# Optimization experiments

Hardware: AMD Instinct MI355X
Metric: run time of the kernel (lower is better)

## Reference

```python
import jax, jax.numpy as jnp
import numpy as np

NEG_SLOPE = 0.1
N, D = 8192, 256


def setup_inputs() -> dict:
    key = jax.random.key(0)
    ks = jax.random.split(key, 7)
    head = jax.random.normal(ks[0], (N, D), dtype=jnp.float32)
    dependent = jax.random.normal(ks[1], (N, D), dtype=jnp.float32)
    alpha = jax.random.uniform(ks[2], (N, N), dtype=jnp.float32)
    # parameters (torch.rand init -> uniform [0,1))
    agg_weight_head = jax.random.uniform(ks[3], (D, D), dtype=jnp.float32)
    agg_weight_dependent = jax.random.uniform(ks[4], (D, D), dtype=jnp.float32)
    comb_weight_head = jax.random.uniform(ks[5], (D, D), dtype=jnp.float32)
    comb_weight_dependent = jax.random.uniform(ks[6], (D, D), dtype=jnp.float32)
    return {
        "head": head, "dependent": dependent, "alpha": alpha,
        "agg_weight_head": agg_weight_head,
        "agg_weight_dependent": agg_weight_dependent,
        "comb_weight_head": comb_weight_head,
        "comb_weight_dependent": comb_weight_dependent,
    }


def reference(head, dependent, alpha, agg_weight_head, agg_weight_dependent,
              comb_weight_head, comb_weight_dependent):
    # Double loop over j != i is equivalent to dense matmuls with the
    # diagonal contribution subtracted:
    #   head_agg[i]  = sum_j alpha[j,i]*head[j] + alpha[i,j]*dependent[j]  (j != i)
    #   dep_agg[i]   = sum_j alpha[i,j]*head[j] + alpha[j,i]*dependent[j]  (j != i)
    diag = jnp.diagonal(alpha)[:, None]                      # [N,1]
    hd_sum = head + dependent                                # [N,D]
    head_agg = alpha.T @ head + alpha @ dependent - diag * hd_sum
    dep_agg = alpha @ head + alpha.T @ dependent - diag * hd_sum
    head_out = jax.nn.leaky_relu(head_agg @ agg_weight_head + head @ comb_weight_head,
                                 negative_slope=NEG_SLOPE)
    dep_out = jax.nn.leaky_relu(dep_agg @ agg_weight_dependent + dependent @ comb_weight_dependent,
                                negative_slope=NEG_SLOPE)
    return (head_out, dep_out)
```

## Files before the change

### kernel.cpp

```cpp
#include <hip/hip_runtime.h>

#define NN 8192
#define DD 256
#define ND_ (NN * DD)

#define NEG_SLOPE 0.1f

typedef _Float16 half8 __attribute__((ext_vector_type(8)));
typedef _Float16 half4 __attribute__((ext_vector_type(4)));
typedef float f32x4 __attribute__((ext_vector_type(4)));
typedef float f32x16 __attribute__((ext_vector_type(16)));

__device__ __forceinline__ void ld_g2l16(const void* g, void* l) {
    __builtin_amdgcn_global_load_lds(
        (const __attribute__((address_space(1))) void*)g,
        (__attribute__((address_space(3))) void*)l, 16, 0, 0);
}

__device__ __forceinline__ unsigned pkhalf2(_Float16 a, _Float16 b) {
    unsigned short ua = __builtin_bit_cast(unsigned short, a);
    unsigned short ub = __builtin_bit_cast(unsigned short, b);
    return (unsigned)ua | ((unsigned)ub << 16);
}

__global__ __launch_bounds__(256, 2)
void prep_split_kernel(const float* __restrict__ h, const float* __restrict__ d,
                       _Float16* __restrict__ uS_hi, _Float16* __restrict__ vS_hi) {
    __shared__ float s_h[64 * 68];
    __shared__ float s_d[64 * 68];
    const int b  = blockIdx.x;
    const int kt = b >> 2;
    const int ct = b & 3;
    const int k0 = kt * 64;
    const int c0 = ct * 64;
    const int t  = threadIdx.x;

#pragma unroll
    for (int e = 0; e < 4; ++e) {
        int idx = e * 256 + t;
        int r   = idx >> 4;
        int c4  = (idx & 15) << 2;
        float4 hv = *(const float4*)&h[(size_t)(k0 + r) * DD + c0 + c4];
        float4 dv = *(const float4*)&d[(size_t)(k0 + r) * DD + c0 + c4];
        *(float4*)&s_h[r * 68 + c4] = hv;
        *(float4*)&s_d[r * 68 + c4] = dv;
    }
    __syncthreads();

#pragma unroll
    for (int e = 0; e < 2; ++e) {
        int idx = e * 256 + t;
        int c   = idx >> 3;
        int seg = idx & 7;
        half8 uh, vh;
#pragma unroll
        for (int m = 0; m < 8; ++m) {
            float hh = s_h[(seg * 8 + m) * 68 + c];
            float dd = s_d[(seg * 8 + m) * 68 + c];
            uh[m] = (_Float16)(hh + dd);
            vh[m] = (_Float16)(hh - dd);
        }
        int    cg   = c0 + c;
        int    kb   = kt * 2 + (seg >> 2);
        int    slot = (seg & 3) ^ ((cg >> 1) & 3);
        size_t go   = (size_t)kb * 8192 + (size_t)cg * 32 + slot * 8;
        *(half8*)&uS_hi[go] = uh;
        *(half8*)&vS_hi[go] = vh;
    }
}

__global__ __launch_bounds__(512, 4)
void agg_mfma_kernel(const float* __restrict__ alpha,
                     const _Float16* __restrict__ uS_hi, const _Float16* __restrict__ vS_hi,
                     _Float16* __restrict__ Pbuf,
                     _Float16* __restrict__ Qbuf) {
    __shared__ __align__(16) unsigned char smem[53248];
    _Float16* sS0  = (_Float16*)smem;
    _Float16* sD0  = (_Float16*)(smem + 5120);
    _Float16* sS1  = (_Float16*)(smem + 10240);
    _Float16* sD1  = (_Float16*)(smem + 15360);
    _Float16* sBu0 = (_Float16*)(smem + 20480);
    _Float16* sBv0 = (_Float16*)(smem + 28672);
    _Float16* sBu1 = (_Float16*)(smem + 36864);
    _Float16* sBv1 = (_Float16*)(smem + 45056);

    const int raw   = blockIdx.x;
    const int khalf = raw & 1;
    const int cb    = (raw >> 3) & 1;
    const int rb    = ((raw >> 1) & 3) | ((raw >> 4) << 2);
    const int I0    = rb * 64;
    const int C0    = cb * 128;
    const int t     = threadIdx.x;
    const int w     = t >> 6;
    const int lane  = t & 63;

    const bool isP = (w < 4);
    const int  cw  = w & 3;

    const _Float16* aP0 = isP ? sS0 : sD0;
    const _Float16* aP1 = isP ? sS1 : sD1;
    const _Float16* b0  = isP ? sBu0 : sBv0;
    const _Float16* b1  = isP ? sBu1 : sBv1;

    f32x16 acc0, acc1;
#pragma unroll
    for (int r = 0; r < 16; ++r) { acc0[r] = 0.f; acc1[r] = 0.f; }

    const int rbase = t & 15;
    const int kp    = (t >> 4) & 15;
    const int dup   = t >> 8;
    const int row0  = rbase + 32 * dup;
    const int lrow  = lane & 31;
    const int lk    = (lane >> 5) << 3;
    const int kbase = khalf * (NN / 2);
    const int c_local = cw * 32 + lrow;

#define LOAD_ALPHA(S, IT)                                                        \
    {                                                                            \
        const int kk0 = kbase + (IT) * 64 + 2 * kp;                              \
        size_t c0off = (size_t)kk0 * NN + I0;                                    \
        S##c00 = alpha[c0off + row0];                                            \
        S##c01 = alpha[c0off + NN + row0];                                       \
        S##c10 = alpha[c0off + row0 + 16];                                       \
        S##c11 = alpha[c0off + NN + row0 + 16];                                  \
        size_t c1off = c0off + (size_t)32 * NN;                                  \
        S##d00 = alpha[c1off + row0];                                            \
        S##d01 = alpha[c1off + NN + row0];                                       \
        S##d10 = alpha[c1off + row0 + 16];                                       \
        S##d11 = alpha[c1off + NN + row0 + 16];                                  \
        S##r00 = *(const float2*)&alpha[(size_t)(I0 + row0) * NN + kk0];         \
        S##r10 = *(const float2*)&alpha[(size_t)(I0 + row0 + 16) * NN + kk0];    \
        S##r01 = *(const float2*)&alpha[(size_t)(I0 + row0) * NN + kk0 + 32];    \
        S##r11 = *(const float2*)&alpha[(size_t)(I0 + row0 + 16) * NN + kk0 + 32]; \
    }

    float Ac00, Ac01, Ac10, Ac11, Ad00, Ad01, Ad10, Ad11;
    float2 Ar00, Ar10, Ar01, Ar11;
    float Bc00, Bc01, Bc10, Bc11, Bd00, Bd01, Bd10, Bd11;
    float2 Br00, Br10, Br01, Br11;
    float Cc00, Cc01, Cc10, Cc11, Cd00, Cd01, Cd10, Cd11;
    float2 Cr00, Cr10, Cr01, Cr11;
    float Nc00, Nc01, Nc10, Nc11, Nd00, Nd01, Nd10, Nd11;
    float2 Nr00, Nr10, Nr01, Nr11;

    LOAD_ALPHA(A, 0)
    LOAD_ALPHA(B, 1)
    LOAD_ALPHA(C, 2)

    for (int it = 0; it < 64; ++it) {
        unsigned su0_0 = pkhalf2((_Float16)(Ac00 + Ar00.x), (_Float16)(Ac01 + Ar00.y));
        unsigned du0_0 = pkhalf2((_Float16)(Ac00 - Ar00.x), (_Float16)(Ac01 - Ar00.y));
        unsigned su1_0 = pkhalf2((_Float16)(Ac10 + Ar10.x), (_Float16)(Ac11 + Ar10.y));
        unsigned du1_0 = pkhalf2((_Float16)(Ac10 - Ar10.x), (_Float16)(Ac11 - Ar10.y));
        unsigned su0_1 = pkhalf2((_Float16)(Ad00 + Ar01.x), (_Float16)(Ad01 + Ar01.y));
        unsigned du0_1 = pkhalf2((_Float16)(Ad00 - Ar01.x), (_Float16)(Ad01 - Ar01.y));
        unsigned su1_1 = pkhalf2((_Float16)(Ad10 + Ar11.x), (_Float16)(Ad11 + Ar11.y));
        unsigned du1_1 = pkhalf2((_Float16)(Ad10 - Ar11.x), (_Float16)(Ad11 - Ar11.y));

        __syncthreads();

        ((unsigned*)sS0)[row0 * 20 + kp]        = su0_0;
        ((unsigned*)sS0)[(row0 + 16) * 20 + kp] = su1_0;
        ((unsigned*)sD0)[row0 * 20 + kp]        = du0_0;
        ((unsigned*)sD0)[(row0 + 16) * 20 + kp] = du1_0;
        ((unsigned*)sS1)[row0 * 20 + kp]        = su0_1;
        ((unsigned*)sS1)[(row0 + 16) * 20 + kp] = su1_1;
        ((unsigned*)sD1)[row0 * 20 + kp]        = du0_1;
        ((unsigned*)sD1)[(row0 + 16) * 20 + kp] = du1_1;

        {
            size_t gb0 = (size_t)(khalf * 128 + it * 2) * 8192 + cb * 4096 +
                         (size_t)(w * 512 + lane * 8);
            ld_g2l16(uS_hi + gb0, (unsigned char*)sBu0 + w * 1024);
            ld_g2l16(vS_hi + gb0, (unsigned char*)sBv0 + w * 1024);
            ld_g2l16(uS_hi + gb0 + 8192, (unsigned char*)sBu1 + w * 1024);
            ld_g2l16(vS_hi + gb0 + 8192, (unsigned char*)sBv1 + w * 1024);
        }
        __builtin_amdgcn_sched_barrier(0);

        LOAD_ALPHA(N, ((it + 3) & 63))
        __builtin_amdgcn_sched_barrier(0);

        asm volatile("s_waitcnt vmcnt(12)" ::: "memory");
        asm volatile("s_waitcnt lgkmcnt(0)" ::: "memory");
        __builtin_amdgcn_s_barrier();
        __builtin_amdgcn_sched_barrier(0);

        __builtin_amdgcn_s_setprio(1);
#pragma unroll
        for (int s = 0; s < 2; ++s) {
            int gd = s * 2 + (lane >> 5);
            int sl = gd ^ ((c_local >> 1) & 3);
            int bi = c_local * 32 + sl * 8;
            half8 aH0 = *(const half8*)&aP0[(lrow) * 40 + s * 16 + lk];
            half8 aH1 = *(const half8*)&aP0[(32 + lrow) * 40 + s * 16 + lk];
            half8 bH  = *(const half8*)&b0[bi];
            acc0 = __builtin_amdgcn_mfma_f32_32x32x16_f16(aH0, bH, acc0, 0, 0, 0);
            acc1 = __builtin_amdgcn_mfma_f32_32x32x16_f16(aH1, bH, acc1, 0, 0, 0);
        }
#pragma unroll
        for (int s = 0; s < 2; ++s) {
            int gd = s * 2 + (lane >> 5);
            int sl = gd ^ ((c_local >> 1) & 3);
            int bi = c_local * 32 + sl * 8;
            half8 aH0 = *(const half8*)&aP1[(lrow) * 40 + s * 16 + lk];
            half8 aH1 = *(const half8*)&aP1[(32 + lrow) * 40 + s * 16 + lk];
            half8 bH  = *(const half8*)&b1[bi];
            acc0 = __builtin_amdgcn_mfma_f32_32x32x16_f16(aH0, bH, acc0, 0, 0, 0);
            acc1 = __builtin_amdgcn_mfma_f32_32x32x16_f16(aH1, bH, acc1, 0, 0, 0);
        }
        __builtin_amdgcn_s_setprio(0);

        Ac00 = Bc00; Ac01 = Bc01; Ac10 = Bc10; Ac11 = Bc11;
        Ad00 = Bd00; Ad01 = Bd01; Ad10 = Bd10; Ad11 = Bd11;
        Ar00 = Br00; Ar10 = Br10; Ar01 = Br01; Ar11 = Br11;
        Bc00 = Cc00; Bc01 = Cc01; Bc10 = Cc10; Bc11 = Cc11;
        Bd00 = Cd00; Bd01 = Cd01; Bd10 = Cd10; Bd11 = Cd11;
        Br00 = Cr00; Br10 = Cr10; Br01 = Cr01; Br11 = Cr11;
        Cc00 = Nc00; Cc01 = Nc01; Cc10 = Nc10; Cc11 = Nc11;
        Cd00 = Nd00; Cd01 = Nd01; Cd10 = Nd10; Cd11 = Nd11;
        Cr00 = Nr00; Cr10 = Nr10; Cr01 = Nr01; Cr11 = Nr11;
    }
#undef LOAD_ALPHA

    _Float16* dst = (isP ? Pbuf : Qbuf) + (size_t)khalf * ND_;
    const int colw = C0 + cw * 32 + (lane & 31);
#pragma unroll
    for (int reg = 0; reg < 16; ++reg) {
        int rr = (reg & 3) + ((reg >> 2) << 3) + ((lane >> 5) << 2);
        dst[(size_t)(I0 + rr) * DD + colw]      = (_Float16)acc0[reg];
        dst[(size_t)(I0 + 32 + rr) * DD + colw] = (_Float16)acc1[reg];
    }
}

__global__ __launch_bounds__(256, 2)
void stageB_kernel(const _Float16* __restrict__ Pbuf, const _Float16* __restrict__ Qbuf,
                   const float* __restrict__ head, const float* __restrict__ dep,
                   const float* __restrict__ alpha,
                   const float* __restrict__ Wah, const float* __restrict__ Wad,
                   const float* __restrict__ Wch, const float* __restrict__ Wcd,
                   float* __restrict__ out) {
    __shared__ float smem2[12544];
    __shared__ float s_dg[64];
    float* s_x  = smem2;
    float* s_y  = smem2 + 2176;
    float* s_w1 = smem2 + 4352;
    float* s_w2 = smem2 + 8448;

    int b   = blockIdx.x;
    int sel = b >> 8;
    int rem = b & 255;
    int rb  = rem >> 1;
    int cb  = rem & 1;
    int I0  = rb * 64;
    int C0  = cb * 128;

    const float* Y  = sel ? dep : head;
    const float* W1 = sel ? Wad : Wah;
    const float* W2 = sel ? Wcd : Wch;
    float* dst = out + sel * ND_;

    int t  = threadIdx.x;
    int rg = t & 15, cg = t >> 4;
    int r0 = rg * 4, c0 = cg * 8;

    if (t < 64) s_dg[t] = alpha[(size_t)(I0 + t) * NN + I0 + t];

    float acc[4][8];
#pragma unroll
    for (int i = 0; i < 4; ++i)
#pragma unroll
        for (int j = 0; j < 8; ++j) acc[i][j] = 0.0f;

    for (int it = 0; it < 8; ++it) {
        int k0 = it * 32;
        __syncthreads();
#pragma unroll
        for (int e = 0; e < 2; ++e) {
            int idx = e * 256 + t;
            int r   = idx >> 3;
            int k4  = (idx & 7) << 2;
            size_t go = (size_t)(I0 + r) * DD + k0 + k4;
            half4 p0 = *(const half4*)&Pbuf[go];
            half4 p1 = *(const half4*)&Pbuf[ND_ + go];
            half4 q0 = *(const half4*)&Qbuf[go];
            half4 q1 = *(const half4*)&Qbuf[ND_ + go];
            float4 hv = *(const float4*)&head[go];
            float4 dv = *(const float4*)&dep[go];
            float dgv = s_dg[r];
            float hj[4] = {hv.x, hv.y, hv.z, hv.w};
            float dj[4] = {dv.x, dv.y, dv.z, dv.w};
#pragma unroll
            for (int j = 0; j < 4; ++j) {
                float Pv = (float)p0[j] + (float)p1[j];
                float Qv = (float)q0[j] + (float)q1[j];
                float uu = hj[j] + dj[j];
                float x  = (sel ? 0.5f * (Pv - Qv) : 0.5f * (Pv + Qv)) - dgv * uu;
                s_x[(k4 + j) * 68 + r] = x;
                s_y[(k4 + j) * 68 + r] = sel ? dj[j] : hj[j];
            }
        }
#pragma unroll
        for (int e = 0; e < 4; ++e) {
            int idx = e * 256 + t;
            int kkk = idx >> 5;
            int c4  = (idx & 31) << 2;
            *(float4*)&s_w1[kkk * 128 + c4] =
                *(const float4*)&W1[(size_t)(k0 + kkk) * DD + C0 + c4];
            *(float4*)&s_w2[kkk * 128 + c4] =
                *(const float4*)&W2[(size_t)(k0 + kkk) * DD + C0 + c4];
        }
        __syncthreads();
#pragma unroll 8
        for (int k = 0; k < 32; ++k) {
            float4 xv = *(const float4*)&s_x[k * 68 + r0];
            float4 yv = *(const float4*)&s_y[k * 68 + r0];
            float4 wa = *(const float4*)&s_w1[k * 128 + c0];
            float4 wb = *(const float4*)&s_w1[k * 128 + c0 + 4];
            float4 wc = *(const float4*)&s_w2[k * 128 + c0];
            float4 wd = *(const float4*)&s_w2[k * 128 + c0 + 4];
            float xs[4]  = {xv.x, xv.y, xv.z, xv.w};
            float ys[4]  = {yv.x, yv.y, yv.z, yv.w};
            float w1s[8] = {wa.x, wa.y, wa.z, wa.w, wb.x, wb.y, wb.z, wb.w};
            float w2s[8] = {wc.x, wc.y, wc.z, wc.w, wd.x, wd.y, wd.z, wd.w};
#pragma unroll
            for (int i = 0; i < 4; ++i)
#pragma unroll
                for (int j = 0; j < 8; ++j)
                    acc[i][j] += xs[i] * w1s[j] + ys[i] * w2s[j];
        }
    }

#pragma unroll
    for (int i = 0; i < 4; ++i) {
#pragma unroll
        for (int jv = 0; jv < 2; ++jv) {
            float4 o;
            float v0 = acc[i][4 * jv + 0];
            float v1 = acc[i][4 * jv + 1];
            float v2 = acc[i][4 * jv + 2];
            float v3 = acc[i][4 * jv + 3];
            o.x = v0 >= 0.0f ? v0 : NEG_SLOPE * v0;
            o.y = v1 >= 0.0f ? v1 : NEG_SLOPE * v1;
            o.z = v2 >= 0.0f ? v2 : NEG_SLOPE * v2;
            o.w = v3 >= 0.0f ? v3 : NEG_SLOPE * v3;
            *(float4*)&dst[(size_t)(I0 + r0 + i) * DD + C0 + c0 + 4 * jv] = o;
        }
    }
}

extern "C" void kernel_launch(void* const* d_in, const int* in_sizes, int n_in,
                              void* d_out, int out_size, void* d_ws, size_t ws_size,
                              hipStream_t stream) {
    const float* head  = (const float*)d_in[0];
    const float* dep   = (const float*)d_in[1];
    const float* alpha = (const float*)d_in[2];
    const float* Wah   = (const float*)d_in[3];
    const float* Wad   = (const float*)d_in[4];
    const float* Wch   = (const float*)d_in[5];
    const float* Wcd   = (const float*)d_in[6];
    float* out = (float*)d_out;

    _Float16* ws    = (_Float16*)d_ws;
    _Float16* uS_hi = ws;
    _Float16* vS_hi = ws + (size_t)ND_;
    _Float16* Pbuf  = ws + (size_t)2 * ND_;
    _Float16* Qbuf  = ws + (size_t)4 * ND_;

    prep_split_kernel<<<512, 256, 0, stream>>>(head, dep, uS_hi, vS_hi);
    agg_mfma_kernel<<<512, 512, 0, stream>>>(alpha, uS_hi, vS_hi, Pbuf, Qbuf);
    stageB_kernel<<<512, 256, 0, stream>>>(Pbuf, Qbuf, head, dep, alpha,
                                           Wah, Wad, Wch, Wcd, out);
}
```

Baseline: 314.8 us.

## Enlarge agg row tile to 128 and split K four ways

The aggregation kernel now covers 128 rows per block instead of 64, using four accumulators per wave so each B tile loaded from LDS feeds more MFMAs. K is split into quarters rather than halves, which doubles the partial P/Q buffers and makes stageB sum four partials. The alpha prefetch depth drops from three iterations ahead to one, with a full vmcnt(0) wait at the top of each iteration. The costs are more LDS per block (73 KB), more registers, less latency hiding on alpha loads, and extra partial-sum traffic through the workspace.

```diff
diff --git a/kernel.cpp b/kernel.cpp
--- a/kernel.cpp
+++ b/kernel.cpp
@@ -74,25 +74,25 @@
                      const _Float16* __restrict__ uS_hi, const _Float16* __restrict__ vS_hi,
                      _Float16* __restrict__ Pbuf,
                      _Float16* __restrict__ Qbuf) {
-    __shared__ __align__(16) unsigned char smem[53248];
+    __shared__ __align__(16) unsigned char smem[73728];
     _Float16* sS0  = (_Float16*)smem;
-    _Float16* sD0  = (_Float16*)(smem + 5120);
-    _Float16* sS1  = (_Float16*)(smem + 10240);
-    _Float16* sD1  = (_Float16*)(smem + 15360);
-    _Float16* sBu0 = (_Float16*)(smem + 20480);
-    _Float16* sBv0 = (_Float16*)(smem + 28672);
-    _Float16* sBu1 = (_Float16*)(smem + 36864);
-    _Float16* sBv1 = (_Float16*)(smem + 45056);
-
-    const int raw   = blockIdx.x;
-    const int khalf = raw & 1;
-    const int cb    = (raw >> 3) & 1;
-    const int rb    = ((raw >> 1) & 3) | ((raw >> 4) << 2);
-    const int I0    = rb * 64;
-    const int C0    = cb * 128;
-    const int t     = threadIdx.x;
-    const int w     = t >> 6;
-    const int lane  = t & 63;
+    _Float16* sD0  = (_Float16*)(smem + 10240);
+    _Float16* sS1  = (_Float16*)(smem + 20480);
+    _Float16* sD1  = (_Float16*)(smem + 30720);
+    _Float16* sBu0 = (_Float16*)(smem + 40960);
+    _Float16* sBv0 = (_Float16*)(smem + 49152);
+    _Float16* sBu1 = (_Float16*)(smem + 57344);
+    _Float16* sBv1 = (_Float16*)(smem + 65536);
+
+    const int raw  = blockIdx.x;
+    const int kq   = raw & 3;
+    const int cb   = (raw >> 2) & 1;
+    const int rb   = raw >> 3;
+    const int I0   = rb * 128;
+    const int C0   = cb * 128;
+    const int t    = threadIdx.x;
+    const int w    = t >> 6;
+    const int lane = t & 63;
 
     const bool isP = (w < 4);
     const int  cw  = w & 3;
@@ -102,74 +102,88 @@
     const _Float16* b0  = isP ? sBu0 : sBv0;
     const _Float16* b1  = isP ? sBu1 : sBv1;
 
-    f32x16 acc0, acc1;
-#pragma unroll
-    for (int r = 0; r < 16; ++r) { acc0[r] = 0.f; acc1[r] = 0.f; }
-
-    const int rbase = t & 15;
+    f32x16 acc0, acc1, acc2, acc3;
+#pragma unroll
+    for (int r = 0; r < 16; ++r) { acc0[r] = 0.f; acc1[r] = 0.f; acc2[r] = 0.f; acc3[r] = 0.f; }
+
+    const int q     = t & 15;
     const int kp    = (t >> 4) & 15;
     const int dup   = t >> 8;
-    const int row0  = rbase + 32 * dup;
+    const int row0  = q + 16 * (4 * dup + 0);
+    const int row1  = q + 16 * (4 * dup + 1);
+    const int row2  = q + 16 * (4 * dup + 2);
+    const int row3  = q + 16 * (4 * dup + 3);
     const int lrow  = lane & 31;
     const int lk    = (lane >> 5) << 3;
-    const int kbase = khalf * (NN / 2);
+    const int kbase = kq * 2048;
     const int c_local = cw * 32 + lrow;
 
-#define LOAD_ALPHA(S, IT)                                                        \
-    {                                                                            \
-        const int kk0 = kbase + (IT) * 64 + 2 * kp;                              \
-        size_t c0off = (size_t)kk0 * NN + I0;                                    \
-        S##c00 = alpha[c0off + row0];                                            \
-        S##c01 = alpha[c0off + NN + row0];                                       \
-        S##c10 = alpha[c0off + row0 + 16];                                       \
-        S##c11 = alpha[c0off + NN + row0 + 16];                                  \
-        size_t c1off = c0off + (size_t)32 * NN;                                  \
-        S##d00 = alpha[c1off + row0];                                            \
-        S##d01 = alpha[c1off + NN + row0];                                       \
-        S##d10 = alpha[c1off + row0 + 16];                                       \
-        S##d11 = alpha[c1off + NN + row0 + 16];                                  \
-        S##r00 = *(const float2*)&alpha[(size_t)(I0 + row0) * NN + kk0];         \
-        S##r10 = *(const float2*)&alpha[(size_t)(I0 + row0 + 16) * NN + kk0];    \
-        S##r01 = *(const float2*)&alpha[(size_t)(I0 + row0) * NN + kk0 + 32];    \
-        S##r11 = *(const float2*)&alpha[(size_t)(I0 + row0 + 16) * NN + kk0 + 32]; \
-    }
-
-    float Ac00, Ac01, Ac10, Ac11, Ad00, Ad01, Ad10, Ad11;
-    float2 Ar00, Ar10, Ar01, Ar11;
-    float Bc00, Bc01, Bc10, Bc11, Bd00, Bd01, Bd10, Bd11;
-    float2 Br00, Br10, Br01, Br11;
-    float Cc00, Cc01, Cc10, Cc11, Cd00, Cd01, Cd10, Cd11;
-    float2 Cr00, Cr10, Cr01, Cr11;
-    float Nc00, Nc01, Nc10, Nc11, Nd00, Nd01, Nd10, Nd11;
-    float2 Nr00, Nr10, Nr01, Nr11;
+#define LOAD_ALPHA(S, IT)                                                          \
+    {                                                                              \
+        const int kk0 = kbase + (IT) * 64 + 2 * kp;                                \
+        size_t z0 = (size_t)kk0 * NN + I0;                                         \
+        size_t z1 = z0 + (size_t)32 * NN;                                          \
+        S##c000 = alpha[z0 + row0];      S##c010 = alpha[z0 + NN + row0];          \
+        S##c001 = alpha[z0 + row1];      S##c011 = alpha[z0 + NN + row1];          \
+        S##c002 = alpha[z0 + row2];      S##c012 = alpha[z0 + NN + row2];          \
+        S##c003 = alpha[z0 + row3];      S##c013 = alpha[z0 + NN + row3];          \
+        S##c100 = alpha[z1 + row0];      S##c110 = alpha[z1 + NN + row0];          \
+        S##c101 = alpha[z1 + row1];      S##c111 = alpha[z1 + NN + row1];          \
+        S##c102 = alpha[z1 + row2];      S##c112 = alpha[z1 + NN + row2];          \
+        S##c103 = alpha[z1 + row3];      S##c113 = alpha[z1 + NN + row3];          \
+        S##r00 = *(const float2*)&alpha[(size_t)(I0 + row0) * NN + kk0];           \
+        S##r01 = *(const float2*)&alpha[(size_t)(I0 + row1) * NN + kk0];           \
+        S##r02 = *(const float2*)&alpha[(size_t)(I0 + row2) * NN + kk0];           \
+        S##r03 = *(const float2*)&alpha[(size_t)(I0 + row3) * NN + kk0];           \
+        S##r10 = *(const float2*)&alpha[(size_t)(I0 + row0) * NN + kk0 + 32];      \
+        S##r11 = *(const float2*)&alpha[(size_t)(I0 + row1) * NN + kk0 + 32];      \
+        S##r12 = *(const float2*)&alpha[(size_t)(I0 + row2) * NN + kk0 + 32];      \
+        S##r13 = *(const float2*)&alpha[(size_t)(I0 + row3) * NN + kk0 + 32];      \
+    }
+
+    float Ac000, Ac010, Ac001, Ac011, Ac002, Ac012, Ac003, Ac013;
+    float Ac100, Ac110, Ac101, Ac111, Ac102, Ac112, Ac103, Ac113;
+    float2 Ar00, Ar01, Ar02, Ar03, Ar10, Ar11, Ar12, Ar13;
+    float Nc000, Nc010, Nc001, Nc011, Nc002, Nc012, Nc003, Nc013;
+    float Nc100, Nc110, Nc101, Nc111, Nc102, Nc112, Nc103, Nc113;
+    float2 Nr00, Nr01, Nr02, Nr03, Nr10, Nr11, Nr12, Nr13;
 
     LOAD_ALPHA(A, 0)
-    LOAD_ALPHA(B, 1)
-    LOAD_ALPHA(C, 2)
-
-    for (int it = 0; it < 64; ++it) {
-        unsigned su0_0 = pkhalf2((_Float16)(Ac00 + Ar00.x), (_Float16)(Ac01 + Ar00.y));
-        unsigned du0_0 = pkhalf2((_Float16)(Ac00 - Ar00.x), (_Float16)(Ac01 - Ar00.y));
-        unsigned su1_0 = pkhalf2((_Float16)(Ac10 + Ar10.x), (_Float16)(Ac11 + Ar10.y));
-        unsigned du1_0 = pkhalf2((_Float16)(Ac10 - Ar10.x), (_Float16)(Ac11 - Ar10.y));
-        unsigned su0_1 = pkhalf2((_Float16)(Ad00 + Ar01.x), (_Float16)(Ad01 + Ar01.y));
-        unsigned du0_1 = pkhalf2((_Float16)(Ad00 - Ar01.x), (_Float16)(Ad01 - Ar01.y));
-        unsigned su1_1 = pkhalf2((_Float16)(Ad10 + Ar11.x), (_Float16)(Ad11 + Ar11.y));
-        unsigned du1_1 = pkhalf2((_Float16)(Ad10 - Ar11.x), (_Float16)(Ad11 - Ar11.y));
+
+    for (int it = 0; it < 32; ++it) {
+        asm volatile("s_waitcnt vmcnt(0)" ::: "memory");
+        __builtin_amdgcn_sched_barrier(0);
+
+        unsigned s00 = pkhalf2((_Float16)(Ac000 + Ar00.x), (_Float16)(Ac010 + Ar00.y));
+        unsigned d00 = pkhalf2((_Float16)(Ac000 - Ar00.x), (_Float16)(Ac010 - Ar00.y));
+        unsigned s01 = pkhalf2((_Float16)(Ac001 + Ar01.x), (_Float16)(Ac011 + Ar01.y));
+        unsigned d01 = pkhalf2((_Float16)(Ac001 - Ar01.x), (_Float16)(Ac011 - Ar01.y));
+        unsigned s02 = pkhalf2((_Float16)(Ac002 + Ar02.x), (_Float16)(Ac012 + Ar02.y));
+        unsigned d02 = pkhalf2((_Float16)(Ac002 - Ar02.x), (_Float16)(Ac012 - Ar02.y));
+        unsigned s03 = pkhalf2((_Float16)(Ac003 + Ar03.x), (_Float16)(Ac013 + Ar03.y));
+        unsigned d03 = pkhalf2((_Float16)(Ac003 - Ar03.x), (_Float16)(Ac013 - Ar03.y));
+        unsigned s10 = pkhalf2((_Float16)(Ac100 + Ar10.x), (_Float16)(Ac110 + Ar10.y));
+        unsigned d10 = pkhalf2((_Float16)(Ac100 - Ar10.x), (_Float16)(Ac110 - Ar10.y));
+        unsigned s11 = pkhalf2((_Float16)(Ac101 + Ar11.x), (_Float16)(Ac111 + Ar11.y));
+        unsigned d11 = pkhalf2((_Float16)(Ac101 - Ar11.x), (_Float16)(Ac111 - Ar11.y));
+        unsigned s12 = pkhalf2((_Float16)(Ac102 + Ar12.x), (_Float16)(Ac112 + Ar12.y));
+        unsigned d12 = pkhalf2((_Float16)(Ac102 - Ar12.x), (_Float16)(Ac112 - Ar12.y));
+        unsigned s13 = pkhalf2((_Float16)(Ac103 + Ar13.x), (_Float16)(Ac113 + Ar13.y));
+        unsigned d13 = pkhalf2((_Float16)(Ac103 - Ar13.x), (_Float16)(Ac113 - Ar13.y));
 
         __syncthreads();
 
-        ((unsigned*)sS0)[row0 * 20 + kp]        = su0_0;
-        ((unsigned*)sS0)[(row0 + 16) * 20 + kp] = su1_0;
-        ((unsigned*)sD0)[row0 * 20 + kp]        = du0_0;
-        ((unsigned*)sD0)[(row0 + 16) * 20 + kp] = du1_0;
-        ((unsigned*)sS1)[row0 * 20 + kp]        = su0_1;
-        ((unsigned*)sS1)[(row0 + 16) * 20 + kp] = su1_1;
-        ((unsigned*)sD1)[row0 * 20 + kp]        = du0_1;
-        ((unsigned*)sD1)[(row0 + 16) * 20 + kp] = du1_1;
+        ((unsigned*)sS0)[row0 * 20 + kp] = s00;  ((unsigned*)sD0)[row0 * 20 + kp] = d00;
+        ((unsigned*)sS0)[row1 * 20 + kp] = s01;  ((unsigned*)sD0)[row1 * 20 + kp] = d01;
+        ((unsigned*)sS0)[row2 * 20 + kp] = s02;  ((unsigned*)sD0)[row2 * 20 + kp] = d02;
+        ((unsigned*)sS0)[row3 * 20 + kp] = s03;  ((unsigned*)sD0)[row3 * 20 + kp] = d03;
+        ((unsigned*)sS1)[row0 * 20 + kp] = s10;  ((unsigned*)sD1)[row0 * 20 + kp] = d10;
+        ((unsigned*)sS1)[row1 * 20 + kp] = s11;  ((unsigned*)sD1)[row1 * 20 + kp] = d11;
+        ((unsigned*)sS1)[row2 * 20 + kp] = s12;  ((unsigned*)sD1)[row2 * 20 + kp] = d12;
+        ((unsigned*)sS1)[row3 * 20 + kp] = s13;  ((unsigned*)sD1)[row3 * 20 + kp] = d13;
 
         {
-            size_t gb0 = (size_t)(khalf * 128 + it * 2) * 8192 + cb * 4096 +
+            size_t gb0 = (size_t)(kq * 64 + it * 2) * 8192 + cb * 4096 +
                          (size_t)(w * 512 + lane * 8);
             ld_g2l16(uS_hi + gb0, (unsigned char*)sBu0 + w * 1024);
             ld_g2l16(vS_hi + gb0, (unsigned char*)sBv0 + w * 1024);
@@ -178,10 +192,10 @@
         }
         __builtin_amdgcn_sched_barrier(0);
 
-        LOAD_ALPHA(N, ((it + 3) & 63))
+        LOAD_ALPHA(N, ((it + 1) & 31))
         __builtin_amdgcn_sched_barrier(0);
 
-        asm volatile("s_waitcnt vmcnt(12)" ::: "memory");
+        asm volatile("s_waitcnt vmcnt(24)" ::: "memory");
         asm volatile("s_waitcnt lgkmcnt(0)" ::: "memory");
         __builtin_amdgcn_s_barrier();
         __builtin_amdgcn_sched_barrier(0);
@@ -192,44 +206,51 @@
             int gd = s * 2 + (lane >> 5);
             int sl = gd ^ ((c_local >> 1) & 3);
             int bi = c_local * 32 + sl * 8;
-            half8 aH0 = *(const half8*)&aP0[(lrow) * 40 + s * 16 + lk];
-            half8 aH1 = *(const half8*)&aP0[(32 + lrow) * 40 + s * 16 + lk];
-            half8 bH  = *(const half8*)&b0[bi];
-            acc0 = __builtin_amdgcn_mfma_f32_32x32x16_f16(aH0, bH, acc0, 0, 0, 0);
-            acc1 = __builtin_amdgcn_mfma_f32_32x32x16_f16(aH1, bH, acc1, 0, 0, 0);
+            half8 bH = *(const half8*)&b0[bi];
+            half8 a0 = *(const half8*)&aP0[(lrow) * 40 + s * 16 + lk];
+            half8 a1 = *(const half8*)&aP0[(32 + lrow) * 40 + s * 16 + lk];
+            half8 a2 = *(const half8*)&aP0[(64 + lrow) * 40 + s * 16 + lk];
+            half8 a3 = *(const half8*)&aP0[(96 + lrow) * 40 + s * 16 + lk];
+            acc0 = __builtin_amdgcn_mfma_f32_32x32x16_f16(a0, bH, acc0, 0, 0, 0);
+            acc1 = __builtin_amdgcn_mfma_f32_32x32x16_f16(a1, bH, acc1, 0, 0, 0);
+            acc2 = __builtin_amdgcn_mfma_f32_32x32x16_f16(a2, bH, acc2, 0, 0, 0);
+            acc3 = __builtin_amdgcn_mfma_f32_32x32x16_f16(a3, bH, acc3, 0, 0, 0);
         }
 #pragma unroll
         for (int s = 0; s < 2; ++s) {
             int gd = s * 2 + (lane >> 5);
             int sl = gd ^ ((c_local >> 1) & 3);
             int bi = c_local * 32 + sl * 8;
-            half8 aH0 = *(const half8*)&aP1[(lrow) * 40 + s * 16 + lk];
-            half8 aH1 = *(const half8*)&aP1[(32 + lrow) * 40 + s * 16 + lk];
-            half8 bH  = *(const half8*)&b1[bi];
-            acc0 = __builtin_amdgcn_mfma_f32_32x32x16_f16(aH0, bH, acc0, 0, 0, 0);
-            acc1 = __builtin_amdgcn_mfma_f32_32x32x16_f16(aH1, bH, acc1, 0, 0, 0);
+            half8 bH = *(const half8*)&b1[bi];
+            half8 a0 = *(const half8*)&aP1[(lrow) * 40 + s * 16 + lk];
+            half8 a1 = *(const half8*)&aP1[(32 + lrow) * 40 + s * 16 + lk];
+            half8 a2 = *(const half8*)&aP1[(64 + lrow) * 40 + s * 16 + lk];
+            half8 a3 = *(const half8*)&aP1[(96 + lrow) * 40 + s * 16 + lk];
+            acc0 = __builtin_amdgcn_mfma_f32_32x32x16_f16(a0, bH, acc0, 0, 0, 0);
+            acc1 = __builtin_amdgcn_mfma_f32_32x32x16_f16(a1, bH, acc1, 0, 0, 0);
+            acc2 = __builtin_amdgcn_mfma_f32_32x32x16_f16(a2, bH, acc2, 0, 0, 0);
+            acc3 = __builtin_amdgcn_mfma_f32_32x32x16_f16(a3, bH, acc3, 0, 0, 0);
         }
         __builtin_amdgcn_s_setprio(0);
 
-        Ac00 = Bc00; Ac01 = Bc01; Ac10 = Bc10; Ac11 = Bc11;
-        Ad00 = Bd00; Ad01 = Bd01; Ad10 = Bd10; Ad11 = Bd11;
-        Ar00 = Br00; Ar10 = Br10; Ar01 = Br01; Ar11 = Br11;
-        Bc00 = Cc00; Bc01 = Cc01; Bc10 = Cc10; Bc11 = Cc11;
-        Bd00 = Cd00; Bd01 = Cd01; Bd10 = Cd10; Bd11 = Cd11;
-        Br00 = Cr00; Br10 = Cr10; Br01 = Cr01; Br11 = Cr11;
-        Cc00 = Nc00; Cc01 = Nc01; Cc10 = Nc10; Cc11 = Nc11;
-        Cd00 = Nd00; Cd01 = Nd01; Cd10 = Nd10; Cd11 = Nd11;
-        Cr00 = Nr00; Cr10 = Nr10; Cr01 = Nr01; Cr11 = Nr11;
+        Ac000 = Nc000; Ac010 = Nc010; Ac001 = Nc001; Ac011 = Nc011;
+        Ac002 = Nc002; Ac012 = Nc012; Ac003 = Nc003; Ac013 = Nc013;
+        Ac100 = Nc100; Ac110 = Nc110; Ac101 = Nc101; Ac111 = Nc111;
+        Ac102 = Nc102; Ac112 = Nc112; Ac103 = Nc103; Ac113 = Nc113;
+        Ar00 = Nr00; Ar01 = Nr01; Ar02 = Nr02; Ar03 = Nr03;
+        Ar10 = Nr10; Ar11 = Nr11; Ar12 = Nr12; Ar13 = Nr13;
     }
 #undef LOAD_ALPHA
 
-    _Float16* dst = (isP ? Pbuf : Qbuf) + (size_t)khalf * ND_;
+    _Float16* dst = (isP ? Pbuf : Qbuf) + (size_t)kq * ND_;
     const int colw = C0 + cw * 32 + (lane & 31);
 #pragma unroll
     for (int reg = 0; reg < 16; ++reg) {
         int rr = (reg & 3) + ((reg >> 2) << 3) + ((lane >> 5) << 2);
-        dst[(size_t)(I0 + rr) * DD + colw]      = (_Float16)acc0[reg];
-        dst[(size_t)(I0 + 32 + rr) * DD + colw] = (_Float16)acc1[reg];
+        dst[(size_t)(I0 + rr) * DD + colw]       = (_Float16)acc0[reg];
+        dst[(size_t)(I0 + 32 + rr) * DD + colw]  = (_Float16)acc1[reg];
+        dst[(size_t)(I0 + 64 + rr) * DD + colw]  = (_Float16)acc2[reg];
+        dst[(size_t)(I0 + 96 + rr) * DD + colw]  = (_Float16)acc3[reg];
     }
 }
 
@@ -283,8 +304,12 @@
             size_t go = (size_t)(I0 + r) * DD + k0 + k4;
             half4 p0 = *(const half4*)&Pbuf[go];
             half4 p1 = *(const half4*)&Pbuf[ND_ + go];
+            half4 p2 = *(const half4*)&Pbuf[2 * (size_t)ND_ + go];
+            half4 p3 = *(const half4*)&Pbuf[3 * (size_t)ND_ + go];
             half4 q0 = *(const half4*)&Qbuf[go];
             half4 q1 = *(const half4*)&Qbuf[ND_ + go];
+            half4 q2 = *(const half4*)&Qbuf[2 * (size_t)ND_ + go];
+            half4 q3 = *(const half4*)&Qbuf[3 * (size_t)ND_ + go];
             float4 hv = *(const float4*)&head[go];
             float4 dv = *(const float4*)&dep[go];
             float dgv = s_dg[r];
@@ -292,8 +317,8 @@
             float dj[4] = {dv.x, dv.y, dv.z, dv.w};
 #pragma unroll
             for (int j = 0; j < 4; ++j) {
-                float Pv = (float)p0[j] + (float)p1[j];
-                float Qv = (float)q0[j] + (float)q1[j];
+                float Pv = ((float)p0[j] + (float)p1[j]) + ((float)p2[j] + (float)p3[j]);
+                float Qv = ((float)q0[j] + (float)q1[j]) + ((float)q2[j] + (float)q3[j]);
                 float uu = hj[j] + dj[j];
                 float x  = (sel ? 0.5f * (Pv - Qv) : 0.5f * (Pv + Qv)) - dgv * uu;
                 s_x[(k4 + j) * 68 + r] = x;
@@ -365,7 +390,7 @@
     _Float16* uS_hi = ws;
     _Float16* vS_hi = ws + (size_t)ND_;
     _Float16* Pbuf  = ws + (size_t)2 * ND_;
-    _Float16* Qbuf  = ws + (size_t)4 * ND_;
+    _Float16* Qbuf  = ws + (size_t)6 * ND_;
 
     prep_split_kernel<<<512, 256, 0, stream>>>(head, dep, uS_hi, vS_hi);
     agg_mfma_kernel<<<512, 512, 0, stream>>>(alpha, uS_hi, vS_hi, Pbuf, Qbuf);
```

New measurement: 353.3 us. 1.12x slower.
